# Kernel optimization log

Hardware: AMD Instinct MI355X
Metric: run time of the kernel (lower is better)

The kernel has to match this reference:

```python
import jax, jax.numpy as jnp
import numpy as np

DIM, N_HEADS, N_KV, HEAD_DIM = 4096, 32, 8, 128
REPEATS = N_HEADS // N_KV
SCALE = HEAD_DIM ** -0.5


def apply_rope(x, offset=0):
    # x: [b, h, l, hd]; rotation convention matches the torch source:
    # out_even = xe*cos + xo*sin, out_odd = -xe*sin + xo*cos, interleaved back.
    hd = x.shape[-1]
    l = x.shape[2]
    freqs = 1.0 / 10000.0 ** (jnp.arange(0, hd, 2, dtype=jnp.float32) / hd)  # [hd/2]
    t = jnp.arange(l, dtype=jnp.float32) + offset
    ang = t[:, None] * freqs[None, :]                     # [l, hd/2]
    sin, cos = jnp.sin(ang), jnp.cos(ang)
    xe, xo = x[..., 0::2], x[..., 1::2]                   # [b,h,l,hd/2]
    out = jnp.stack([xe * cos + xo * sin, -xe * sin + xo * cos], axis=-1)
    return out.reshape(x.shape)


def setup_inputs() -> dict:
    key = jax.random.key(0)
    ks = jax.random.split(key, 5)
    b, l = 1, 2048
    x = jax.random.normal(ks[0], (b, l, DIM), dtype=jnp.float32)
    # additive causal mask: 0 on/below diagonal, -1e9 above
    neg = jnp.full((l, l), -1e9, dtype=jnp.float32)
    mask = jnp.triu(neg, k=1)
    wq = jax.random.normal(ks[1], (N_HEADS * HEAD_DIM, DIM), dtype=jnp.float32) * 0.02
    wk = jax.random.normal(ks[2], (N_KV * HEAD_DIM, DIM), dtype=jnp.float32) * 0.02
    wv = jax.random.normal(ks[3], (N_KV * HEAD_DIM, DIM), dtype=jnp.float32) * 0.02
    wo = jax.random.normal(ks[4], (DIM, N_HEADS * HEAD_DIM), dtype=jnp.float32) * 0.02
    return {"x": x, "mask": mask, "wq": wq, "wk": wk, "wv": wv, "wo": wo}


def reference(x, mask, wq, wk, wv, wo):
    b, l, d = x.shape
    q = (x @ wq.T).reshape(b, l, N_HEADS, HEAD_DIM).transpose(0, 2, 1, 3)  # [b,H,l,hd]
    k = (x @ wk.T).reshape(b, l, N_KV, HEAD_DIM).transpose(0, 2, 1, 3)     # [b,Hk,l,hd]
    v = (x @ wv.T).reshape(b, l, N_KV, HEAD_DIM).transpose(0, 2, 1, 3)
    # GQA repeat (head = kv_head*repeats + r, same as torch cat+view)
    k = jnp.repeat(k, REPEATS, axis=1)
    v = jnp.repeat(v, REPEATS, axis=1)
    q = apply_rope(q)
    k = apply_rope(k)
    atn = jnp.einsum('bhqd,bhkd->bhqk', q * SCALE, k) + mask
    atn = jax.nn.softmax(atn.astype(jnp.float32), axis=-1).astype(q.dtype)
    out = jnp.einsum('bhqk,bhkd->bhqd', atn, v)
    out = out.transpose(0, 2, 1, 3).reshape(b, l, -1)
    return (out @ wo.T, k, v)
```

## Files before the change

### kernel.cpp

```cpp
#include <hip/hip_runtime.h>
#include <stdint.h>

#define L_SEQ  2048
#define NHEAD  32
#define NKV    8
#define HD     128
#define DIM    4096
#define KVDIM  1024
#define QKVS   6144
#define SCALE  0.08838834764831845f
#define LOG2E  1.4426950408889634f
#define SM_OFF 12.0f

typedef __attribute__((ext_vector_type(8))) short bf16x8;
typedef __attribute__((ext_vector_type(4))) float f32x4;

__device__ __forceinline__ unsigned short f2bf(float f) {
    unsigned u = __float_as_uint(f);
    u = (u + 0x7FFFu + ((u >> 16) & 1u)) >> 16;
    return (unsigned short)u;
}
__device__ __forceinline__ float bf2f(unsigned short h) {
    return __uint_as_float(((unsigned)h) << 16);
}
__device__ __forceinline__ void gload_lds16(const void* g, void* l) {
    __builtin_amdgcn_global_load_lds(
        (const __attribute__((address_space(1))) unsigned int*)g,
        (__attribute__((address_space(3))) unsigned int*)l, 16, 0, 0);
}

__global__ void cvt_f32_bf16(const float* __restrict__ in, unsigned short* __restrict__ out, int n4) {
    int i = blockIdx.x * blockDim.x + threadIdx.x;
    int stride = gridDim.x * blockDim.x;
    for (; i < n4; i += stride) {
        float4 v = ((const float4*)in)[i];
        ushort4 o;
        o.x = f2bf(v.x); o.y = f2bf(v.y); o.z = f2bf(v.z); o.w = f2bf(v.w);
        ((ushort4*)out)[i] = o;
    }
}

__global__ void rope_table(float2* __restrict__ rt) {
    int i = blockIdx.x * blockDim.x + threadIdx.x;
    if (i >= L_SEQ * 64) return;
    int l = i >> 6, f = i & 63;
    float freq = powf(10000.0f, -(float)f / 64.0f);
    float ang  = (float)l * freq;
    rt[i] = make_float2(cosf(ang), sinf(ang));
}

__global__ void rope_apply(unsigned short* __restrict__ X, const float2* __restrict__ rt,
                           int log2H, int strideShorts, float mul) {
    int i = blockIdx.x * blockDim.x + threadIdx.x;
    int f  = i & 63;
    int hh = (i >> 6) & ((1 << log2H) - 1);
    int l  = i >> (6 + log2H);
    if (l >= L_SEQ) return;
    float2 cs = rt[(l << 6) + f];
    size_t base = (size_t)l * strideShorts + (hh << 7);
    float xe = bf2f(X[base + 2 * f]);
    float xo = bf2f(X[base + 2 * f + 1]);
    X[base + 2 * f]     = f2bf((xe * cs.x + xo * cs.y) * mul);
    X[base + 2 * f + 1] = f2bf((-xe * cs.y + xo * cs.x) * mul);
}

__global__ void kv_out(const unsigned short* __restrict__ KVp,
                       float* __restrict__ KO, float* __restrict__ VO) {
    int i = blockIdx.x * blockDim.x + threadIdx.x;
    if (i >= L_SEQ * KVDIM) return;
    int d  = i & 127;
    int h8 = (i >> 7) & 7;
    int l  = i >> 10;
    float kv = bf2f(KVp[(size_t)l * QKVS + h8 * HD + d]);
    float vv = bf2f(KVp[(size_t)l * QKVS + KVDIM + h8 * HD + d]);
#pragma unroll
    for (int r = 0; r < 4; ++r) {
        int h = h8 * 4 + r;
        KO[((size_t)h * L_SEQ + l) * HD + d] = kv;
        VO[((size_t)h * L_SEQ + l) * HD + d] = vv;
    }
}

__global__ void vtrans(const unsigned short* __restrict__ KVp, unsigned short* __restrict__ VT) {
    __shared__ unsigned short t[32][33];
    int lt = blockIdx.x * 32;
    int h8 = blockIdx.y >> 2;
    int dt = (blockIdx.y & 3) * 32;
    int tx = threadIdx.x & 31, ty = threadIdx.x >> 5;
#pragma unroll
    for (int yy = ty; yy < 32; yy += 8)
        t[yy][tx] = KVp[(size_t)(lt + yy) * QKVS + KVDIM + h8 * HD + dt + tx];
    __syncthreads();
#pragma unroll
    for (int yy = ty; yy < 32; yy += 8)
        VT[(size_t)(h8 * HD + dt + yy) * L_SEQ + lt + tx] = t[tx][yy];
}

template <typename OT>
__global__ __launch_bounds__(512, 2) void gemm_8ph(const unsigned short* __restrict__ A,
                                                   const unsigned short* __restrict__ B,
                                                   OT* __restrict__ C, int N, int K) {
    __shared__ __align__(16) char L[131072];
    const int tid = threadIdx.x;
    const int w = tid >> 6, lane = tid & 63;
    const int gx = gridDim.x;
    const int nwg = gx * gridDim.y;
    const int orig = blockIdx.y * gx + blockIdx.x;
    const int swz = (orig & 7) * (nwg >> 3) + (orig >> 3);
    const int m0 = (swz / gx) * 256, n0 = (swz % gx) * 256;
    const int wr = (w >> 2) & 1;
    const int wc = w & 3;
    const int lr = lane & 15, lg = lane >> 4;
    const int NKT = K >> 6;

    auto stageA = [&](int slot, int half, int kt) {
#pragma unroll
        for (int c = 0; c < 2; ++c) {
            int rl = half * 128 + w * 16 + c * 8;
            int r  = rl + (lane >> 3);
            int cg = (lane & 7) ^ (((r >> 2) & 1) << 1);
            gload_lds16(A + (size_t)(m0 + r) * K + kt * 64 + cg * 8,
                        L + slot * 32768 + rl * 128);
        }
    };
    auto stageB = [&](int slot, int half, int kt) {
#pragma unroll
        for (int c = 0; c < 2; ++c) {
            int rl = half * 128 + w * 16 + c * 8;
            int r  = rl + (lane >> 3);
            int cg = (lane & 7) ^ (((r >> 2) & 1) << 1);
            gload_lds16(B + (size_t)(n0 + r) * K + kt * 64 + cg * 8,
                        L + 65536 + slot * 32768 + rl * 128);
        }
    };

    const f32x4 fz = {0.f, 0.f, 0.f, 0.f};
    f32x4 acc[8][4];
#pragma unroll
    for (int m = 0; m < 8; ++m)
#pragma unroll
        for (int n = 0; n < 4; ++n) acc[m][n] = fz;

    stageA(0, 0, 0); stageA(0, 1, 0); stageB(0, 0, 0); stageB(0, 1, 0);
    if (NKT > 1) { stageB(1, 0, 1); stageB(1, 1, 1); }
    asm volatile("s_waitcnt vmcnt(4)" ::: "memory");
    __builtin_amdgcn_s_barrier();

    bf16x8 bfrag[4][2];
    for (int kt = 0; kt < NKT; ++kt) {
        const int s = kt & 1;
        const char* Abase = L + s * 32768;
        const char* Bbase = L + 65536 + s * 32768;
#pragma unroll
        for (int q = 0; q < 4; ++q) {
            bf16x8 af[2][2];
#pragma unroll
            for (int mm = 0; mm < 2; ++mm)
#pragma unroll
                for (int kk = 0; kk < 2; ++kk) {
                    int r = wr * 128 + (q * 2 + mm) * 16 + lr;
                    int b = (kk * 64 + lg * 16) ^ (((r >> 2) & 1) << 5);
                    af[mm][kk] = *(const bf16x8*)(Abase + r * 128 + b);
                }
            if (q == 0) {
#pragma unroll
                for (int n = 0; n < 4; ++n)
#pragma unroll
                    for (int kk = 0; kk < 2; ++kk) {
                        int r = wc * 64 + n * 16 + lr;
                        int b = (kk * 64 + lg * 16) ^ (((r >> 2) & 1) << 5);
                        bfrag[n][kk] = *(const bf16x8*)(Bbase + r * 128 + b);
                    }
            }
            if (q == 0 && kt + 1 < NKT) stageA(s ^ 1, 0, kt + 1);
            if (q == 1 && kt + 1 < NKT) stageA(s ^ 1, 1, kt + 1);
            if (q == 2 && kt + 2 < NKT) stageB(s, 0, kt + 2);
            if (q == 3) {
                if (kt + 2 < NKT) stageB(s, 1, kt + 2);
                asm volatile("s_waitcnt vmcnt(4)" ::: "memory");
            }
            __builtin_amdgcn_s_barrier();
            asm volatile("s_waitcnt lgkmcnt(0)" ::: "memory");
            __builtin_amdgcn_sched_barrier(0);
            __builtin_amdgcn_s_setprio(1);
#pragma unroll
            for (int mm = 0; mm < 2; ++mm)
#pragma unroll
                for (int n = 0; n < 4; ++n)
#pragma unroll
                    for (int kk = 0; kk < 2; ++kk)
                        acc[q * 2 + mm][n] = __builtin_amdgcn_mfma_f32_16x16x32_bf16(
                            af[mm][kk], bfrag[n][kk], acc[q * 2 + mm][n], 0, 0, 0);
            __builtin_amdgcn_s_setprio(0);
            __builtin_amdgcn_s_barrier();
        }
    }
#pragma unroll
    for (int m = 0; m < 8; ++m) {
        int mrow = m0 + wr * 128 + m * 16 + lg * 4;
#pragma unroll
        for (int n = 0; n < 4; ++n) {
            int ncol = n0 + wc * 64 + n * 16 + lr;
#pragma unroll
            for (int r = 0; r < 4; ++r) {
                float v = acc[m][n][r];
                if constexpr (sizeof(OT) == 2) C[(size_t)(mrow + r) * N + ncol] = f2bf(v);
                else                           C[(size_t)(mrow + r) * N + ncol] = v;
            }
        }
    }
}

__global__ __launch_bounds__(128) void attn_fwd(const unsigned short* __restrict__ Q,
                                                const unsigned short* __restrict__ KVp,
                                                const unsigned short* __restrict__ VT,
                                                unsigned short* __restrict__ AO) {
    __shared__ __align__(16) unsigned short Ks[64 * 128];
    __shared__ __align__(16) unsigned short Vs[128 * 64];
    __shared__ __align__(16) unsigned short P[2][2][16][64];
    const int tid = threadIdx.x, w = tid >> 6, lane = tid & 63;
    const int idx = blockIdx.x;
    const int h8  = idx & 7;
    const int h   = (h8 << 2) + ((idx >> 3) & 3);
    const int u   = idx >> 5;
    const int t   = u & 7, quart = u >> 3;
    const int qb  = (quart == 0) ? 31 - t : (quart == 1) ? 16 + t
                  : (quart == 2) ? 15 - t : t;
    const int lr = lane & 15, lg = lane >> 4;
    const int r0 = qb * 64 + w * 32;

    bf16x8 qf[2][4];
#pragma unroll
    for (int f = 0; f < 2; ++f) {
        const unsigned short* qrow = Q + (size_t)(r0 + f * 16 + lr) * QKVS + h * HD + lg * 8;
#pragma unroll
        for (int kd = 0; kd < 4; ++kd) qf[f][kd] = *(const bf16x8*)(qrow + kd * 32);
    }

    bf16x8 ones;
#pragma unroll
    for (int z = 0; z < 8; ++z) ones[z] = (short)0x3F80;

    const f32x4 fz = {0.f, 0.f, 0.f, 0.f};
    f32x4 o[2][9];
#pragma unroll
    for (int f = 0; f < 2; ++f)
#pragma unroll
        for (int nd = 0; nd < 9; ++nd) o[f][nd] = fz;

    const int nkv = qb + 1;
    for (int kv = 0; kv < nkv; ++kv) {
        const int kv0 = kv * 64;
#pragma unroll
        for (int c = 0; c < 8; ++c) {
            int krow = w * 32 + c * 4 + (lane >> 4);
            int kcg  = (lane & 15) ^ (krow & 7);
            gload_lds16(KVp + (size_t)(kv0 + krow) * QKVS + h8 * HD + kcg * 8,
                        Ks + (w * 32 + c * 4) * 128);
            int vrow = w * 64 + c * 8 + (lane >> 3);
            int vcg  = (lane & 7) ^ (vrow & 7);
            gload_lds16(VT + (size_t)(h8 * HD + vrow) * L_SEQ + kv0 + vcg * 8,
                        Vs + (w * 64 + c * 8) * 64);
        }
        __syncthreads();
        f32x4 s[2][4];
#pragma unroll
        for (int f = 0; f < 2; ++f)
#pragma unroll
            for (int ni = 0; ni < 4; ++ni) s[f][ni] = fz;
        __builtin_amdgcn_s_setprio(1);
#pragma unroll
        for (int ni = 0; ni < 4; ++ni) {
            bf16x8 kf[4];
#pragma unroll
            for (int kd = 0; kd < 4; ++kd)
                kf[kd] = *(const bf16x8*)(Ks + (ni * 16 + lr) * 128 +
                                          (((kd * 4 + lg) ^ (lr & 7)) * 8));
#pragma unroll
            for (int f = 0; f < 2; ++f)
#pragma unroll
                for (int kd = 0; kd < 4; ++kd)
                    s[f][ni] = __builtin_amdgcn_mfma_f32_16x16x32_bf16(qf[f][kd], kf[kd], s[f][ni], 0, 0, 0);
        }
        __builtin_amdgcn_s_setprio(0);
#pragma unroll
        for (int f = 0; f < 2; ++f) {
            const int rbase = r0 + f * 16;
            const bool need_mask = (kv0 + 63) > rbase;
#pragma unroll
            for (int ni = 0; ni < 4; ++ni)
#pragma unroll
                for (int rr = 0; rr < 4; ++rr) {
                    float p = __builtin_amdgcn_exp2f(s[f][ni][rr] - SM_OFF);
                    if (need_mask) {
                        int col = kv0 + ni * 16 + lr;
                        int row = rbase + lg * 4 + rr;
                        p = (col > row) ? 0.f : p;
                    }
                    s[f][ni][rr] = p;
                }
            char* Pb = (char*)&P[w][f][0][0];
#pragma unroll
            for (int ni = 0; ni < 4; ni += 2)
#pragma unroll
                for (int rr = 0; rr < 4; ++rr) {
                    unsigned pk;
                    asm("v_cvt_pk_bf16_f32 %0, %1, %2" : "=v"(pk) : "v"(s[f][ni][rr]), "v"(s[f][ni + 1][rr]));
                    const int row = lg * 4 + rr;
                    const int sw = (row & 7) << 4;
                    *(unsigned short*)(Pb + ((row * 128 + (ni * 16 + lr) * 2) ^ sw)) = (unsigned short)pk;
                    *(unsigned short*)(Pb + ((row * 128 + ((ni + 1) * 16 + lr) * 2) ^ sw)) =
                        (unsigned short)(pk >> 16);
                }
        }
        bf16x8 pa[2][2];
        const int swr = (lr & 7) << 4;
#pragma unroll
        for (int f = 0; f < 2; ++f) {
            const char* Pb = (const char*)&P[w][f][0][0];
#pragma unroll
            for (int ks = 0; ks < 2; ++ks)
                pa[f][ks] = *(const bf16x8*)(Pb + ((lr * 128 + ks * 64 + lg * 16) ^ swr));
        }
        __builtin_amdgcn_s_setprio(1);
#pragma unroll
        for (int nd = 0; nd < 8; ++nd) {
            bf16x8 vf[2];
#pragma unroll
            for (int ks = 0; ks < 2; ++ks)
                vf[ks] = *(const bf16x8*)(Vs + (nd * 16 + lr) * 64 +
                                          (((ks * 4 + lg) ^ (lr & 7)) * 8));
#pragma unroll
            for (int f = 0; f < 2; ++f)
#pragma unroll
                for (int ks = 0; ks < 2; ++ks)
                    o[f][nd] = __builtin_amdgcn_mfma_f32_16x16x32_bf16(pa[f][ks], vf[ks], o[f][nd], 0, 0, 0);
        }
#pragma unroll
        for (int f = 0; f < 2; ++f)
#pragma unroll
            for (int ks = 0; ks < 2; ++ks)
                o[f][8] = __builtin_amdgcn_mfma_f32_16x16x32_bf16(pa[f][ks], ones, o[f][8], 0, 0, 0);
        __builtin_amdgcn_s_setprio(0);
        __syncthreads();
    }
#pragma unroll
    for (int f = 0; f < 2; ++f) {
        float inv[4];
#pragma unroll
        for (int rr = 0; rr < 4; ++rr) inv[rr] = 1.0f / o[f][8][rr];
#pragma unroll
        for (int nd = 0; nd < 8; ++nd)
#pragma unroll
            for (int rr = 0; rr < 4; ++rr) {
                int row = r0 + f * 16 + lg * 4 + rr;
                AO[(size_t)row * DIM + h * HD + nd * 16 + lr] = f2bf(o[f][nd][rr] * inv[rr]);
            }
    }
}

extern "C" void kernel_launch(void* const* d_in, const int* in_sizes, int n_in,
                              void* d_out, int out_size, void* d_ws, size_t ws_size,
                              hipStream_t stream) {
    (void)in_sizes; (void)n_in; (void)out_size; (void)ws_size;
    const float* x  = (const float*)d_in[0];
    const float* wq = (const float*)d_in[2];
    const float* wk = (const float*)d_in[3];
    const float* wv = (const float*)d_in[4];
    const float* wo = (const float*)d_in[5];

    float* out = (float*)d_out;
    float* KO  = out + (size_t)L_SEQ * DIM;
    float* VO  = KO + (size_t)NHEAD * L_SEQ * HD;

    char* ws = (char*)d_ws;
    const size_t MB = 1024 * 1024;
    unsigned short* xb   = (unsigned short*)(ws);
    unsigned short* wqb  = (unsigned short*)(ws + 16 * MB);
    unsigned short* wkvb = (unsigned short*)(ws + 48 * MB);
    unsigned short* qkvp = (unsigned short*)(ws + 64 * MB);
    unsigned short* vtb  = (unsigned short*)(ws + 88 * MB);
    float2*         rt   = (float2*)(ws + 92 * MB);
    unsigned short* aob  = xb;
    unsigned short* wob  = wqb;
    unsigned short* kvp  = qkvp + KVDIM * 4;

    cvt_f32_bf16<<<2048, 256, 0, stream>>>(x,  xb,  L_SEQ * DIM / 4);
    cvt_f32_bf16<<<2048, 256, 0, stream>>>(wq, wqb, DIM * DIM / 4);
    cvt_f32_bf16<<<2048, 256, 0, stream>>>(wk, wkvb, KVDIM * DIM / 4);
    cvt_f32_bf16<<<2048, 256, 0, stream>>>(wv, wkvb + (size_t)KVDIM * DIM, KVDIM * DIM / 4);
    rope_table<<<(L_SEQ * 64) / 256, 256, 0, stream>>>(rt);

    gemm_8ph<unsigned short><<<dim3(QKVS / 256, L_SEQ / 256), 512, 0, stream>>>(xb, wqb, qkvp, QKVS, DIM);
    cvt_f32_bf16<<<2048, 256, 0, stream>>>(wo, wob, DIM * DIM / 4);

    rope_apply<<<(L_SEQ * NHEAD * 64) / 256, 256, 0, stream>>>(qkvp, rt, 5, QKVS, SCALE * LOG2E);
    rope_apply<<<(L_SEQ * NKV * 64) / 256, 256, 0, stream>>>(kvp, rt, 3, QKVS, 1.0f);

    kv_out<<<(L_SEQ * KVDIM) / 256, 256, 0, stream>>>(kvp, KO, VO);
    vtrans<<<dim3(L_SEQ / 32, 32), 256, 0, stream>>>(kvp, vtb);

    attn_fwd<<<1024, 128, 0, stream>>>(qkvp, kvp, vtb, aob);

    gemm_8ph<float><<<dim3(DIM / 256, L_SEQ / 256), 512, 0, stream>>>(aob, wob, out, DIM, DIM);
}
```

Before: 387.9 us.

## Split-K the output projection GEMM and widen LDS XOR swizzle

```diff
diff --git a/kernel.cpp b/kernel.cpp
--- a/kernel.cpp
+++ b/kernel.cpp
@@ -37,6 +37,17 @@
         ushort4 o;
         o.x = f2bf(v.x); o.y = f2bf(v.y); o.z = f2bf(v.z); o.w = f2bf(v.w);
         ((ushort4*)out)[i] = o;
+    }
+}
+
+__global__ void addf32(float* __restrict__ out, const float* __restrict__ p, int n4) {
+    int i = blockIdx.x * blockDim.x + threadIdx.x;
+    int stride = gridDim.x * blockDim.x;
+    for (; i < n4; i += stride) {
+        float4 a = ((const float4*)out)[i];
+        float4 b = ((const float4*)p)[i];
+        a.x += b.x; a.y += b.y; a.z += b.z; a.w += b.w;
+        ((float4*)out)[i] = a;
     }
 }
 
@@ -99,7 +110,8 @@
 template <typename OT>
 __global__ __launch_bounds__(512, 2) void gemm_8ph(const unsigned short* __restrict__ A,
                                                    const unsigned short* __restrict__ B,
-                                                   OT* __restrict__ C, int N, int K) {
+                                                   OT* __restrict__ C0, OT* __restrict__ C1,
+                                                   int N, int K, int klen) {
     __shared__ __align__(16) char L[131072];
     const int tid = threadIdx.x;
     const int w = tid >> 6, lane = tid & 63;
@@ -108,18 +120,20 @@
     const int orig = blockIdx.y * gx + blockIdx.x;
     const int swz = (orig & 7) * (nwg >> 3) + (orig >> 3);
     const int m0 = (swz / gx) * 256, n0 = (swz % gx) * 256;
+    const int kbase = blockIdx.z * klen;
+    OT* __restrict__ C = blockIdx.z ? C1 : C0;
     const int wr = (w >> 2) & 1;
     const int wc = w & 3;
     const int lr = lane & 15, lg = lane >> 4;
-    const int NKT = K >> 6;
+    const int NKT = klen >> 6;
 
     auto stageA = [&](int slot, int half, int kt) {
 #pragma unroll
         for (int c = 0; c < 2; ++c) {
             int rl = half * 128 + w * 16 + c * 8;
             int r  = rl + (lane >> 3);
-            int cg = (lane & 7) ^ (((r >> 2) & 1) << 1);
-            gload_lds16(A + (size_t)(m0 + r) * K + kt * 64 + cg * 8,
+            int cg = (lane & 7) ^ (r & 7);
+            gload_lds16(A + (size_t)(m0 + r) * K + kbase + kt * 64 + cg * 8,
                         L + slot * 32768 + rl * 128);
         }
     };
@@ -128,8 +142,8 @@
         for (int c = 0; c < 2; ++c) {
             int rl = half * 128 + w * 16 + c * 8;
             int r  = rl + (lane >> 3);
-            int cg = (lane & 7) ^ (((r >> 2) & 1) << 1);
-            gload_lds16(B + (size_t)(n0 + r) * K + kt * 64 + cg * 8,
+            int cg = (lane & 7) ^ (r & 7);
+            gload_lds16(B + (size_t)(n0 + r) * K + kbase + kt * 64 + cg * 8,
                         L + 65536 + slot * 32768 + rl * 128);
         }
     };
@@ -146,6 +160,7 @@
     asm volatile("s_waitcnt vmcnt(4)" ::: "memory");
     __builtin_amdgcn_s_barrier();
 
+    const int swb = (lr & 7) << 4;
     bf16x8 bfrag[4][2];
     for (int kt = 0; kt < NKT; ++kt) {
         const int s = kt & 1;
@@ -159,7 +174,7 @@
 #pragma unroll
                 for (int kk = 0; kk < 2; ++kk) {
                     int r = wr * 128 + (q * 2 + mm) * 16 + lr;
-                    int b = (kk * 64 + lg * 16) ^ (((r >> 2) & 1) << 5);
+                    int b = (kk * 64 + lg * 16) ^ swb;
                     af[mm][kk] = *(const bf16x8*)(Abase + r * 128 + b);
                 }
             if (q == 0) {
@@ -168,7 +183,7 @@
 #pragma unroll
                     for (int kk = 0; kk < 2; ++kk) {
                         int r = wc * 64 + n * 16 + lr;
-                        int b = (kk * 64 + lg * 16) ^ (((r >> 2) & 1) << 5);
+                        int b = (kk * 64 + lg * 16) ^ swb;
                         bfrag[n][kk] = *(const bf16x8*)(Bbase + r * 128 + b);
                     }
             }
@@ -384,6 +399,7 @@
     unsigned short* aob  = xb;
     unsigned short* wob  = wqb;
     unsigned short* kvp  = qkvp + KVDIM * 4;
+    float*          pko  = (float*)(ws + 48 * MB);
 
     cvt_f32_bf16<<<2048, 256, 0, stream>>>(x,  xb,  L_SEQ * DIM / 4);
     cvt_f32_bf16<<<2048, 256, 0, stream>>>(wq, wqb, DIM * DIM / 4);
@@ -391,7 +407,8 @@
     cvt_f32_bf16<<<2048, 256, 0, stream>>>(wv, wkvb + (size_t)KVDIM * DIM, KVDIM * DIM / 4);
     rope_table<<<(L_SEQ * 64) / 256, 256, 0, stream>>>(rt);
 
-    gemm_8ph<unsigned short><<<dim3(QKVS / 256, L_SEQ / 256), 512, 0, stream>>>(xb, wqb, qkvp, QKVS, DIM);
+    gemm_8ph<unsigned short><<<dim3(QKVS / 256, L_SEQ / 256, 1), 512, 0, stream>>>(
+        xb, wqb, qkvp, qkvp, QKVS, DIM, DIM);
     cvt_f32_bf16<<<2048, 256, 0, stream>>>(wo, wob, DIM * DIM / 4);
 
     rope_apply<<<(L_SEQ * NHEAD * 64) / 256, 256, 0, stream>>>(qkvp, rt, 5, QKVS, SCALE * LOG2E);
@@ -402,5 +419,7 @@
 
     attn_fwd<<<1024, 128, 0, stream>>>(qkvp, kvp, vtb, aob);
 
-    gemm_8ph<float><<<dim3(DIM / 256, L_SEQ / 256), 512, 0, stream>>>(aob, wob, out, DIM, DIM);
-}
+    gemm_8ph<float><<<dim3(DIM / 256, L_SEQ / 256, 2), 512, 0, stream>>>(
+        aob, wob, out, pko, DIM, DIM, DIM / 2);
+    addf32<<<2048, 256, 0, stream>>>(out, pko, L_SEQ * DIM / 4);
+}
```

After: 345.9 us. -10.8%, faster.
